# Kernel optimization log

Hardware: AMD Instinct MI355X
Metric: run time of the kernel (lower is better)

The kernel has to match this reference:

```python
import jax, jax.numpy as jnp
import numpy as np

EPS = 1e-6      # mLSTM normalizer epsilon
LN_EPS = 1e-5   # LayerNorm epsilon (equinox default)
S, E, NH = 2048, 1024, 8
DH = E // NH


def setup_inputs() -> dict:
    key = jax.random.key(0)
    ks = jax.random.split(key, 7)
    q = jax.random.normal(ks[0], (S, E), jnp.float32)
    k = jax.random.normal(ks[1], (S, E), jnp.float32)
    v = jax.random.normal(ks[2], (S, E), jnp.float32)
    # Gate projections: Linear(3E -> NH). Module inits weights to zero; we use
    # small random weights so the S x S gate structure is data-dependent and the
    # full math path is exercised. Biases follow the module's init scheme.
    igate_w = 0.02 * jax.random.normal(ks[3], (NH, 3 * E), jnp.float32)
    igate_b = jnp.linspace(3.0, 6.0, NH, dtype=jnp.float32)
    fgate_w = 0.02 * jax.random.normal(ks[4], (NH, 3 * E), jnp.float32)
    fgate_b = jnp.sqrt(jnp.float32(0.1)) * jax.random.normal(ks[5], (NH,), jnp.float32)
    ln_w = jnp.ones((E,), jnp.float32)  # outnorm weight (use_bias=False)
    return {"q": q, "k": k, "v": v, "igate_w": igate_w, "igate_b": igate_b,
            "fgate_w": fgate_w, "fgate_b": fgate_b, "ln_w": ln_w}


def _mlstm_forward(q, k, v, igate_w, igate_b, fgate_w, fgate_b, ln_w):
    s, e = q.shape
    nh = igate_b.shape[0]
    dh = e // nh
    # gate preactivations from concatenated q,k,v: [S, 3E] @ [3E, NH] -> [NH, S]
    x = jnp.concatenate([q, k, v], axis=1)
    ig = (x @ igate_w.T + igate_b).T            # [NH, S]
    fg = (x @ fgate_w.T + fgate_b).T            # [NH, S]
    # split heads: [NH, S, DH]
    qh = q.reshape(s, nh, dh).transpose(1, 0, 2)
    kh = k.reshape(s, nh, dh).transpose(1, 0, 2)
    vh = v.reshape(s, nh, dh).transpose(1, 0, 2)
    # log forget gates and cumulative sums (with leading zero)
    logf = jax.nn.log_sigmoid(fg)                                   # [NH, S]
    cs = jnp.concatenate([jnp.zeros((nh, 1), logf.dtype),
                          jnp.cumsum(logf, axis=1)], axis=1)        # [NH, S+1]
    # log_fg_matrix[h,i,j] = cs[h,i+1] - cs[h,j+1], masked to causal
    dlog = cs[:, 1:, None] - cs[:, None, 1:]                        # [NH, S, S]
    mask = jnp.tril(jnp.ones((s, s), dtype=bool))
    log_fg_matrix = jnp.where(mask, dlog, -jnp.inf)
    # log D = log forget decay + input gate preact (per source position j)
    log_D = log_fg_matrix + ig[:, None, :]                          # [NH, S, S]
    max_log_D = jnp.max(log_D, axis=-1, keepdims=True)              # row-wise stabilization
    D = jnp.exp(log_D - max_log_D)
    qk = jnp.einsum("hsd,htd->hst", qh, kh) / jnp.sqrt(jnp.float32(dh))
    C = qk * D
    normalizer = jnp.maximum(jnp.abs(C.sum(axis=-1, keepdims=True)), jnp.exp(-max_log_D))
    h = jnp.einsum("hst,htd->hsd", C / (normalizer + EPS), vh)      # [NH, S, DH]
    h = h.transpose(1, 0, 2).reshape(s, e)
    # outnorm: LayerNorm over embedding dim, weight only (no bias)
    mu = h.mean(axis=-1, keepdims=True)
    var = ((h - mu) ** 2).mean(axis=-1, keepdims=True)
    return (h - mu) / jnp.sqrt(var + LN_EPS) * ln_w


def reference(q, k, v, igate_w, igate_b, fgate_w, fgate_b, ln_w):
    return _mlstm_forward(q, k, v, igate_w, igate_b, fgate_w, fgate_b, ln_w)
```

## Files before the change

kernel.cpp:

```cpp
#include <hip/hip_runtime.h>
#include <hip/hip_bf16.h>
#include <math.h>

#define S_LEN 2048
#define E_DIM 1024
#define NHEAD 8
#define DHEAD 128
#define MEPS 1e-6f
#define LNEPS 1e-5f
#define TASKS_PER_HEAD 61

typedef __bf16 bf16x8 __attribute__((ext_vector_type(8)));
typedef __bf16 bf16x4 __attribute__((ext_vector_type(4)));
typedef float f32x4 __attribute__((ext_vector_type(4)));
typedef float f32x16 __attribute__((ext_vector_type(16)));

__device__ __host__ inline int ns_of(int qg) { return (4 * qg + 13) / 10; }

__device__ inline void split8(const float* x, bf16x8& hi, bf16x8& lo) {
#pragma unroll
  for (int e = 0; e < 8; ++e) {
    float v = x[e];
    __bf16 h = (__bf16)v;
    hi[e] = h;
    lo[e] = (__bf16)(v - (float)h);
  }
}

__device__ inline int cvtpk(float a, float b) {
  int d;
  asm("v_cvt_pk_bf16_f32 %0, %1, %2" : "=v"(d) : "v"(a), "v"(b));
  return d;
}

__global__ __launch_bounds__(256) void convw_kernel(
    const float* __restrict__ k, const float* __restrict__ v,
    const float* __restrict__ igw, const float* __restrict__ fgw,
    __bf16* __restrict__ KfH, __bf16* __restrict__ KfL, __bf16* __restrict__ VT,
    __bf16* __restrict__ WfH, __bf16* __restrict__ WfL) {
  __shared__ float Kl[32][132], Vl[32][132];
  int t = threadIdx.x;
  if (blockIdx.x >= 512) {
    int slot = (blockIdx.x - 512) * 256 + t;
    int f = slot >> 6, l = slot & 63;
    int c = l & 15;
    int koff = f * 32 + (l >> 4) * 8;
    const float* wrow = (c < 8) ? (igw + c * 3072) : (fgw + (c - 8) * 3072);
    float buf[8];
#pragma unroll
    for (int e = 0; e < 8; ++e) buf[e] = wrow[koff + e];
    bf16x8 fh, fl; split8(buf, fh, fl);
    *(bf16x8*)(WfH + (size_t)slot * 8) = fh;
    *(bf16x8*)(WfL + (size_t)slot * 8) = fl;
    return;
  }
  int h = blockIdx.x >> 6, kvt = blockIdx.x & 63;
  int kvbase = kvt * 32;
#pragma unroll
  for (int it = 0; it < 4; ++it) {
    int fid = it * 256 + t;
    int r = fid >> 5, c4 = (fid & 31) * 4;
    *(float4*)&Kl[r][c4] = *(const float4*)(k + (size_t)(kvbase + r) * E_DIM + h * DHEAD + c4);
    *(float4*)&Vl[r][c4] = *(const float4*)(v + (size_t)(kvbase + r) * E_DIM + h * DHEAD + c4);
  }
  __syncthreads();
  size_t tb = (size_t)(h * 64 + kvt) * 4096;
#pragma unroll
  for (int it = 0; it < 2; ++it) {
    int slot = it * 256 + t;
    int f = slot >> 6, l = slot & 63;
    int l31 = l & 31, hi = l >> 5;
    {
      float buf[8];
#pragma unroll
      for (int e = 0; e < 8; ++e) buf[e] = Kl[l31][f * 16 + hi * 8 + e];
      bf16x8 fh, fl; split8(buf, fh, fl);
      *(bf16x8*)(KfH + tb + (size_t)slot * 8) = fh;
      *(bf16x8*)(KfL + tb + (size_t)slot * 8) = fl;
    }
    {
      int dt = f >> 1, kch = f & 1;
      bf16x8 fh;
#pragma unroll
      for (int e = 0; e < 8; ++e) fh[e] = (__bf16)Vl[kch * 16 + hi * 8 + e][dt * 32 + l31];
      *(bf16x8*)(VT + tb + (size_t)slot * 8) = fh;
    }
  }
}

__global__ __launch_bounds__(256) void gates_mfma_kernel(
    const float* __restrict__ q, const float* __restrict__ k, const float* __restrict__ v,
    const __bf16* __restrict__ WfH, const __bf16* __restrict__ WfL,
    float* __restrict__ gpart) {
  int rb = blockIdx.x >> 3;
  int ks = blockIdx.x & 7;
  int r0 = rb * 64;
  int tid = threadIdx.x, wave = tid >> 6, lane = tid & 63;
  int l15 = lane & 15, hi = lane >> 4;
  __shared__ char Xl[64 * 512];

  f32x4 cacc = (f32x4){0.f, 0.f, 0.f, 0.f};
  for (int ch = 0; ch < 3; ++ch) {
    int kb = ks * 384 + ch * 128;
    __syncthreads();
#pragma unroll
    for (int it = 0; it < 8; ++it) {
      int fid = it * 256 + tid;
      int row = fid >> 5, c4 = (fid & 31) * 4;
      int kk = kb + c4;
      const float* src = (kk < 1024) ? (q + (size_t)(r0 + row) * 1024 + kk)
                       : (kk < 2048) ? (k + (size_t)(r0 + row) * 1024 + (kk - 1024))
                                     : (v + (size_t)(r0 + row) * 1024 + (kk - 2048));
      float4 xv = *(const float4*)src;
      *(float4*)(Xl + ((row * 512 + c4 * 4) ^ ((row & 7) << 4))) = xv;
    }
    __syncthreads();
#pragma unroll
    for (int kc = 0; kc < 4; ++kc) {
      int row = wave * 16 + l15;
      int base = row * 512 + (kc * 32 + hi * 8) * 4;
      int x = (row & 7) << 4;
      float buf[8];
      *(float4*)&buf[0] = *(const float4*)(Xl + (base ^ x));
      *(float4*)&buf[4] = *(const float4*)(Xl + ((base + 16) ^ x));
      bf16x8 ah, al; split8(buf, ah, al);
      int gkc = ks * 12 + ch * 4 + kc;
      bf16x8 bh = *(const bf16x8*)(WfH + (size_t)(gkc * 64 + lane) * 8);
      bf16x8 bl = *(const bf16x8*)(WfL + (size_t)(gkc * 64 + lane) * 8);
      cacc = __builtin_amdgcn_mfma_f32_16x16x32_bf16(ah, bh, cacc, 0, 0, 0);
      cacc = __builtin_amdgcn_mfma_f32_16x16x32_bf16(ah, bl, cacc, 0, 0, 0);
      cacc = __builtin_amdgcn_mfma_f32_16x16x32_bf16(al, bh, cacc, 0, 0, 0);
    }
  }
#pragma unroll
  for (int rg = 0; rg < 4; ++rg) {
    int r = r0 + wave * 16 + hi * 4 + rg;
    gpart[((size_t)ks * S_LEN + r) * 16 + l15] = cacc[rg];
  }
}

__global__ __launch_bounds__(256) void combine_ls_kernel(
    const float* __restrict__ gpart, const float* __restrict__ igb,
    const float* __restrict__ fgb, float* __restrict__ ig, double* __restrict__ ls) {
  int t = blockIdx.x * 256 + threadIdx.x;
  int r = t >> 4, c = t & 15;
  float s = 0.f;
#pragma unroll
  for (int ks = 0; ks < 8; ++ks) s += gpart[((size_t)ks * S_LEN + r) * 16 + c];
  if (c < 8) {
    ig[c * S_LEN + r] = s + igb[c];
  } else {
    double x = (double)(s + fgb[c - 8]);
    ls[(c - 8) * S_LEN + r] = fmin(x, 0.0) - log1p(exp(-fabs(x)));
  }
}

__global__ void scan_kernel(const float* __restrict__ ig, const double* __restrict__ ls,
                            double* __restrict__ g, double* __restrict__ Mv,
                            float* __restrict__ rexpv) {
  int h = blockIdx.x;
  int lane = threadIdx.x;
  double cs0[32];
  const double* lsp = ls + h * S_LEN + lane * 32;
  double run = 0.0;
#pragma unroll
  for (int e = 0; e < 32; ++e) { run += lsp[e]; cs0[e] = run; }
  double incl = run;
#pragma unroll
  for (int off = 1; off < 64; off <<= 1) {
    double nb = __shfl_up(incl, off);
    if (lane >= off) incl += nb;
  }
  double base = __shfl_up(incl, 1);
  if (lane == 0) base = 0.0;
#pragma unroll
  for (int e = 0; e < 32; ++e) cs0[e] += base;

  const float* igp = ig + h * S_LEN + lane * 32;
  double gv[32];
#pragma unroll
  for (int e = 0; e < 32; ++e) {
    gv[e] = (double)igp[e] - cs0[e];
    g[h * S_LEN + lane * 32 + e] = gv[e];
  }
  double pm = -INFINITY;
#pragma unroll
  for (int e = 0; e < 32; ++e) { pm = fmax(pm, gv[e]); gv[e] = pm; }
  double inclm = pm;
#pragma unroll
  for (int off = 1; off < 64; off <<= 1) {
    double nb = __shfl_up(inclm, off);
    if (lane >= off) inclm = fmax(inclm, nb);
  }
  double basem = __shfl_up(inclm, 1);
  if (lane == 0) basem = -INFINITY;
#pragma unroll
  for (int e = 0; e < 32; ++e) {
    double Mi = fmax(basem, gv[e]);
    Mv[h * S_LEN + lane * 32 + e] = Mi;
    rexpv[h * S_LEN + lane * 32 + e] = __expf(-(float)(cs0[e] + Mi));
  }
}

__global__ __launch_bounds__(256) void rebase_kernel(
    const double* __restrict__ g, const double* __restrict__ Mv,
    float* __restrict__ gq, float* __restrict__ Mq) {
  const double L2E = 1.4426950408889634;
  int b = blockIdx.x;
  int h = b >> 4, qg = b & 15;
  int tid = threadIdx.x;
  double base = Mv[h * S_LEN + qg * 128];
#pragma unroll
  for (int it = 0; it < 8; ++it) {
    int j = it * 256 + tid;
    gq[(size_t)(h * 16 + qg) * S_LEN + j] = (float)((g[h * S_LEN + j] - base) * L2E);
  }
  if (tid < 128) {
    int i = qg * 128 + tid;
    Mq[h * S_LEN + i] = (float)((Mv[h * S_LEN + i] - base) * L2E);
  }
}

__global__ __launch_bounds__(256, 2) void attn_kernel(
    const float* __restrict__ q,
    const __bf16* __restrict__ KfH, const __bf16* __restrict__ KfL,
    const __bf16* __restrict__ VT,
    const float* __restrict__ gq, const float* __restrict__ Mq,
    __bf16* __restrict__ part, float* __restrict__ bpart) {
  int rem = blockIdx.x;
  int qg = 15, preLow = 0, ns = 1;
  for (int qq = 15; qq >= 0; --qq) {
    int n = ns_of(qq);
    if (rem < 8 * n) { qg = qq; ns = n; break; }
    rem -= 8 * n;
  }
  for (int qq = 0; qq < qg; ++qq) preLow += ns_of(qq);
  int h = rem & 7;
  int split = rem >> 3;
  int T = 4 * qg + 4;
  int kb_lo = (split * T) / ns;
  int kb_hi = ((split + 1) * T) / ns;
  int Tq = kb_hi - kb_lo;
  int tid = threadIdx.x, wave = tid >> 6, lane = tid & 63;
  int l31 = lane & 31, hi = lane >> 5;
  const float scale = 0.08838834764831845f;

  __shared__ char smem[49152];

  int qrow = qg * 128 + wave * 32 + l31;
  bf16x8 qfh[8], qfl[8];
  {
    const float* qp = q + (size_t)qrow * E_DIM + h * DHEAD + hi * 8;
#pragma unroll
    for (int kch = 0; kch < 8; ++kch) {
      float buf[8];
      *(float4*)&buf[0] = *(const float4*)(qp + kch * 16);
      *(float4*)&buf[4] = *(const float4*)(qp + kch * 16 + 4);
#pragma unroll
      for (int e = 0; e < 8; ++e) buf[e] *= scale;
      split8(buf, qfh[kch], qfl[kch]);
    }
  }
  float Mreg = Mq[h * S_LEN + qrow];
  const float* gqh = gq + (size_t)(h * 16 + qg) * S_LEN;

  f32x16 acc[4];
#pragma unroll
  for (int dt = 0; dt < 4; ++dt) acc[dt] = (f32x16)(0.f);
  float bacc = 0.f;

  size_t laneoff = (size_t)lane * 8;
  auto STAGE = [&](int kb, int buf) {
    size_t tb = (size_t)(h * 64 + kb) * 4096;
    char* lb = smem + buf * 24576;
#pragma unroll
    for (int i = 0; i < 6; ++i) {
      int c = wave * 6 + i;
      const __bf16* src;
      if (c < 8)       src = KfH + tb + (size_t)c * 512 + laneoff;
      else if (c < 16) src = KfL + tb + (size_t)(c - 8) * 512 + laneoff;
      else             src = VT  + tb + (size_t)(c - 16) * 512 + laneoff;
      __builtin_amdgcn_global_load_lds(
          (const __attribute__((address_space(1))) void*)src,
          (__attribute__((address_space(3))) void*)(lb + c * 1024), 16, 0, 0);
    }
  };

  if (Tq > 0) STAGE(kb_lo, 0);
  int cur = 0;
  for (int t = 0; t < Tq; ++t) {
    int kb = kb_lo + t;
    asm volatile("s_waitcnt vmcnt(0)" ::: "memory");
    __builtin_amdgcn_sched_barrier(0);
    asm volatile("s_barrier" ::: "memory");
    if (t + 1 < Tq) STAGE(kb + 1, cur ^ 1);

    int qrelw = qg * 128 + wave * 32 - kb * 32;
    if (qrelw + 31 >= 0) {
      char* lb = smem + cur * 24576;
      int qrel = qrelw + l31;
      float4 g4[4];
#pragma unroll
      for (int c = 0; c < 4; ++c) g4[c] = *(const float4*)(gqh + kb * 32 + 8 * c + 4 * hi);
      f32x16 sA = (f32x16)(0.f), sB = (f32x16)(0.f), sC = (f32x16)(0.f);
      __builtin_amdgcn_s_setprio(1);
#pragma unroll
      for (int kch = 0; kch < 8; ++kch) {
        bf16x8 kh = *(const bf16x8*)(lb + kch * 1024 + lane * 16);
        bf16x8 kl = *(const bf16x8*)(lb + 8192 + kch * 1024 + lane * 16);
        sA = __builtin_amdgcn_mfma_f32_32x32x16_bf16(kh, qfh[kch], sA, 0, 0, 0);
        sB = __builtin_amdgcn_mfma_f32_32x32x16_bf16(kl, qfh[kch], sB, 0, 0, 0);
        sC = __builtin_amdgcn_mfma_f32_32x32x16_bf16(kh, qfl[kch], sC, 0, 0, 0);
      }
      __builtin_amdgcn_s_setprio(0);
      float p[16];
      float bp0 = 0.f, bp1 = 0.f, bp2 = 0.f, bp3 = 0.f;
      if (qrelw >= 31) {
#pragma unroll
        for (int rg = 0; rg < 16; ++rg) {
          float sv = sA[rg] + sB[rg] + sC[rg];
          p[rg] = sv * exp2f(((const float*)&g4[rg >> 2])[rg & 3] - Mreg);
          if ((rg & 3) == 0) bp0 += p[rg];
          else if ((rg & 3) == 1) bp1 += p[rg];
          else if ((rg & 3) == 2) bp2 += p[rg];
          else bp3 += p[rg];
        }
      } else {
#pragma unroll
        for (int rg = 0; rg < 16; ++rg) {
          int J = (rg & 3) + 8 * (rg >> 2) + 4 * hi;
          float sv = sA[rg] + sB[rg] + sC[rg];
          float w = sv * exp2f(((const float*)&g4[rg >> 2])[rg & 3] - Mreg);
          p[rg] = (J <= qrel) ? w : 0.f;
          if ((rg & 3) == 0) bp0 += p[rg];
          else if ((rg & 3) == 1) bp1 += p[rg];
          else if ((rg & 3) == 2) bp2 += p[rg];
          else bp3 += p[rg];
        }
      }
      bacc += (bp0 + bp1) + (bp2 + bp3);
#pragma unroll
      for (int kch = 0; kch < 2; ++kch) {
        const float* pp = p + kch * 8;
        int a0 = cvtpk(pp[0], pp[1]);
        int a1 = cvtpk(pp[2], pp[3]);
        int a2 = cvtpk(pp[4], pp[5]);
        int a3 = cvtpk(pp[6], pp[7]);
        asm("v_permlane32_swap_b32 %0, %1" : "+v"(a0), "+v"(a2));
        asm("v_permlane32_swap_b32 %0, %1" : "+v"(a1), "+v"(a3));
        union { int w[4]; bf16x8 v; } pb;
        pb.w[0] = a0; pb.w[1] = a1; pb.w[2] = a2; pb.w[3] = a3;
        __builtin_amdgcn_s_setprio(1);
#pragma unroll
        for (int dt = 0; dt < 4; ++dt) {
          bf16x8 va = *(const bf16x8*)(lb + 16384 + (dt * 2 + kch) * 1024 + lane * 16);
          acc[dt] = __builtin_amdgcn_mfma_f32_32x32x16_bf16(va, pb.v, acc[dt], 0, 0, 0);
        }
        __builtin_amdgcn_s_setprio(0);
      }
    }
    cur ^= 1;
  }

  {
    int x = __float_as_int(bacc), y = x;
    asm("v_permlane32_swap_b32 %0, %1" : "+v"(x), "+v"(y));
    float bfull = __int_as_float(x) + __int_as_float(y);
    int task = h * TASKS_PER_HEAD + preLow + split;
    if (lane < 32) bpart[task * 128 + wave * 32 + lane] = bfull;

    __syncthreads();
    char* Tls = smem + wave * 8704;
#pragma unroll
    for (int dt = 0; dt < 4; ++dt)
#pragma unroll
      for (int rgq = 0; rgq < 4; ++rgq) {
        bf16x4 pk;
        pk[0] = (__bf16)acc[dt][rgq * 4 + 0];
        pk[1] = (__bf16)acc[dt][rgq * 4 + 1];
        pk[2] = (__bf16)acc[dt][rgq * 4 + 2];
        pk[3] = (__bf16)acc[dt][rgq * 4 + 3];
        int d0 = dt * 32 + rgq * 8 + hi * 4;
        *(bf16x4*)(Tls + l31 * 272 + d0 * 2) = pk;
      }
    __syncthreads();
    __bf16* pp = part + (size_t)task * 16384;
#pragma unroll
    for (int it = 0; it < 8; ++it) {
      int qr = it * 4 + (lane >> 4);
      int chunk = lane & 15;
      bf16x8 vrow = *(const bf16x8*)(Tls + qr * 272 + chunk * 16);
      *(bf16x8*)(pp + ((size_t)(wave * 32 + qr) * 128 + chunk * 8)) = vrow;
    }
  }
}

__global__ __launch_bounds__(256) void cln_kernel(
    const __bf16* __restrict__ part, const float* __restrict__ bpart,
    const float* __restrict__ rexpv, const float* __restrict__ lnw,
    float* __restrict__ out) {
  int b = blockIdx.x;
  int qg = b >> 4, slab = b & 15;
  int ns = ns_of(qg);
  int preLow = 0;
  for (int qq = 0; qq < qg; ++qq) preLow += ns_of(qq);
  int tid = threadIdx.x;
  int tokl = tid >> 5;
  int j = tid & 31;
  int qv = slab * 8 + tokl;
  int tok = qg * 128 + qv;
  int h = j >> 2;
  int d0 = (j & 3) * 32;
  int task0 = h * TASKS_PER_HEAD + preLow;

  float a[32];
#pragma unroll
  for (int i = 0; i < 32; ++i) a[i] = 0.f;
  float bb = 0.f;
  for (int s = 0; s < ns; ++s) {
    const __bf16* pp = part + (size_t)(task0 + s) * 16384 + qv * 128 + d0;
#pragma unroll
    for (int c = 0; c < 4; ++c) {
      bf16x8 xv = *(const bf16x8*)(pp + c * 8);
#pragma unroll
      for (int e = 0; e < 8; ++e) a[c * 8 + e] += (float)xv[e];
    }
    bb += bpart[(task0 + s) * 128 + qv];
  }
  float norm = fmaxf(fabsf(bb), rexpv[h * S_LEN + tok]) + MEPS;
  float inv = 1.f / norm;
  float sum = 0.f, sq = 0.f;
#pragma unroll
  for (int i = 0; i < 32; ++i) {
    a[i] *= inv;
    sum += a[i];
    sq += a[i] * a[i];
  }
#pragma unroll
  for (int off = 1; off < 32; off <<= 1) {
    sum += __shfl_xor(sum, off);
    sq  += __shfl_xor(sq, off);
  }
  float mu = sum * (1.f / E_DIM);
  float var = sq * (1.f / E_DIM) - mu * mu;
  float rstd = rsqrtf(var + LNEPS);
  float* dst = out + (size_t)tok * E_DIM + j * 32;
  const float* wsrc = lnw + j * 32;
#pragma unroll
  for (int c = 0; c < 8; ++c) {
    float4 w = *(const float4*)(wsrc + c * 4);
    float4 o;
    o.x = (a[c * 4 + 0] - mu) * rstd * w.x;
    o.y = (a[c * 4 + 1] - mu) * rstd * w.y;
    o.z = (a[c * 4 + 2] - mu) * rstd * w.z;
    o.w = (a[c * 4 + 3] - mu) * rstd * w.w;
    *(float4*)(dst + c * 4) = o;
  }
}

extern "C" void kernel_launch(void* const* d_in, const int* in_sizes, int n_in,
                              void* d_out, int out_size, void* d_ws, size_t ws_size,
                              hipStream_t stream) {
  const float* q   = (const float*)d_in[0];
  const float* k   = (const float*)d_in[1];
  const float* v   = (const float*)d_in[2];
  const float* igw = (const float*)d_in[3];
  const float* igb = (const float*)d_in[4];
  const float* fgw = (const float*)d_in[5];
  const float* fgb = (const float*)d_in[6];
  const float* lnw = (const float*)d_in[7];
  float* out = (float*)d_out;

  const size_t MB = 1024 * 1024;
  char* base = (char*)d_ws;
  float*  ig    = (float*)(base + 0);
  float*  rexpv = (float*)(base + 64 * 1024);
  float*  Mq    = (float*)(base + 128 * 1024);
  float*  bpart = (float*)(base + 192 * 1024);
  double* ls    = (double*)(base + 704 * 1024);
  double* g64   = (double*)(base + 832 * 1024);
  double* M64   = (double*)(base + 960 * 1024);
  __bf16* WfH   = (__bf16*)(base + 1088 * 1024);
  __bf16* WfL   = (__bf16*)(base + 1184 * 1024);
  float*  gq    = (float*)(base + 1536 * 1024);
  __bf16* KfH   = (__bf16*)(base + 3 * MB);
  __bf16* KfL   = (__bf16*)(base + 7 * MB);
  __bf16* VT    = (__bf16*)(base + 11 * MB);
  __bf16* part  = (__bf16*)(base + 15 * MB);
  float*  gpart = (float*)(base + 31 * MB);

  int nblocks = 8 * TASKS_PER_HEAD;

  convw_kernel<<<dim3(536), dim3(256), 0, stream>>>(k, v, igw, fgw, KfH, KfL, VT, WfH, WfL);
  gates_mfma_kernel<<<dim3(256), dim3(256), 0, stream>>>(q, k, v, WfH, WfL, gpart);
  combine_ls_kernel<<<dim3(128), dim3(256), 0, stream>>>(gpart, igb, fgb, ig, ls);
  scan_kernel<<<dim3(NHEAD), dim3(64), 0, stream>>>(ig, ls, g64, M64, rexpv);
  rebase_kernel<<<dim3(128), dim3(256), 0, stream>>>(g64, M64, gq, Mq);
  attn_kernel<<<dim3(nblocks), dim3(256), 0, stream>>>(q, KfH, KfL, VT, gq, Mq, part, bpart);
  cln_kernel<<<dim3(256), dim3(256), 0, stream>>>(part, bpart, rexpv, lnw, out);
}
```

Before: 77.05 us.

## Fuse scan and rebase kernels and increase attention key-split granularity

Merges the per-head prefix scan and the per-query-group rebase into one kernel that keeps cumulative sums and running maxima in shared memory, dropping a launch and the double-precision global round trip. It also changes the split-count formula so the attention kernel uses more tasks per head, raising parallelism at the cost of more partial results to combine. The partial buffer offset is moved to make room. The fused kernel runs only 8 blocks writing all gq rows, which may serialize work that was previously spread over 128 blocks.

```diff
diff --git a/kernel.cpp b/kernel.cpp
--- a/kernel.cpp
+++ b/kernel.cpp
@@ -8,14 +8,14 @@
 #define DHEAD 128
 #define MEPS 1e-6f
 #define LNEPS 1e-5f
-#define TASKS_PER_HEAD 61
+#define TASKS_PER_HEAD 72
 
 typedef __bf16 bf16x8 __attribute__((ext_vector_type(8)));
 typedef __bf16 bf16x4 __attribute__((ext_vector_type(4)));
 typedef float f32x4 __attribute__((ext_vector_type(4)));
 typedef float f32x16 __attribute__((ext_vector_type(16)));
 
-__device__ __host__ inline int ns_of(int qg) { return (4 * qg + 13) / 10; }
+__device__ __host__ inline int ns_of(int qg) { return (4 * qg + 11) / 8; }
 
 __device__ inline void split8(const float* x, bf16x8& hi, bf16x8& lo) {
 #pragma unroll
@@ -155,69 +155,73 @@
   }
 }
 
-__global__ void scan_kernel(const float* __restrict__ ig, const double* __restrict__ ls,
-                            double* __restrict__ g, double* __restrict__ Mv,
-                            float* __restrict__ rexpv) {
+__global__ __launch_bounds__(256) void scanreb_kernel(
+    const float* __restrict__ ig, const double* __restrict__ ls,
+    float* __restrict__ gq, float* __restrict__ Mq, float* __restrict__ rexpv) {
   int h = blockIdx.x;
-  int lane = threadIdx.x;
-  double cs0[32];
-  const double* lsp = ls + h * S_LEN + lane * 32;
-  double run = 0.0;
-#pragma unroll
-  for (int e = 0; e < 32; ++e) { run += lsp[e]; cs0[e] = run; }
-  double incl = run;
-#pragma unroll
-  for (int off = 1; off < 64; off <<= 1) {
-    double nb = __shfl_up(incl, off);
-    if (lane >= off) incl += nb;
-  }
-  double base = __shfl_up(incl, 1);
-  if (lane == 0) base = 0.0;
-#pragma unroll
-  for (int e = 0; e < 32; ++e) cs0[e] += base;
-
-  const float* igp = ig + h * S_LEN + lane * 32;
-  double gv[32];
-#pragma unroll
-  for (int e = 0; e < 32; ++e) {
-    gv[e] = (double)igp[e] - cs0[e];
-    g[h * S_LEN + lane * 32 + e] = gv[e];
-  }
-  double pm = -INFINITY;
-#pragma unroll
-  for (int e = 0; e < 32; ++e) { pm = fmax(pm, gv[e]); gv[e] = pm; }
-  double inclm = pm;
-#pragma unroll
-  for (int off = 1; off < 64; off <<= 1) {
-    double nb = __shfl_up(inclm, off);
-    if (lane >= off) inclm = fmax(inclm, nb);
-  }
-  double basem = __shfl_up(inclm, 1);
-  if (lane == 0) basem = -INFINITY;
-#pragma unroll
-  for (int e = 0; e < 32; ++e) {
-    double Mi = fmax(basem, gv[e]);
-    Mv[h * S_LEN + lane * 32 + e] = Mi;
-    rexpv[h * S_LEN + lane * 32 + e] = __expf(-(float)(cs0[e] + Mi));
-  }
-}
-
-__global__ __launch_bounds__(256) void rebase_kernel(
-    const double* __restrict__ g, const double* __restrict__ Mv,
-    float* __restrict__ gq, float* __restrict__ Mq) {
+  int tid = threadIdx.x;
+  __shared__ double Lg[2048];
+  __shared__ double Lcs[2048];
+  __shared__ double LM[2048];
+
+  if (tid < 64) {
+    int lane = tid;
+    double cs0[32];
+    const double* lsp = ls + h * S_LEN + lane * 32;
+    double run = 0.0;
+#pragma unroll
+    for (int e = 0; e < 32; ++e) { run += lsp[e]; cs0[e] = run; }
+    double incl = run;
+#pragma unroll
+    for (int off = 1; off < 64; off <<= 1) {
+      double nb = __shfl_up(incl, off);
+      if (lane >= off) incl += nb;
+    }
+    double base = __shfl_up(incl, 1);
+    if (lane == 0) base = 0.0;
+#pragma unroll
+    for (int e = 0; e < 32; ++e) cs0[e] += base;
+
+    const float* igp = ig + h * S_LEN + lane * 32;
+    double gv[32];
+#pragma unroll
+    for (int e = 0; e < 32; ++e) {
+      gv[e] = (double)igp[e] - cs0[e];
+      Lg[lane * 32 + e] = gv[e];
+      Lcs[lane * 32 + e] = cs0[e];
+    }
+    double pm = -INFINITY;
+#pragma unroll
+    for (int e = 0; e < 32; ++e) { pm = fmax(pm, gv[e]); gv[e] = pm; }
+    double inclm = pm;
+#pragma unroll
+    for (int off = 1; off < 64; off <<= 1) {
+      double nb = __shfl_up(inclm, off);
+      if (lane >= off) inclm = fmax(inclm, nb);
+    }
+    double basem = __shfl_up(inclm, 1);
+    if (lane == 0) basem = -INFINITY;
+#pragma unroll
+    for (int e = 0; e < 32; ++e) LM[lane * 32 + e] = fmax(basem, gv[e]);
+  }
+  __syncthreads();
+
   const double L2E = 1.4426950408889634;
-  int b = blockIdx.x;
-  int h = b >> 4, qg = b & 15;
-  int tid = threadIdx.x;
-  double base = Mv[h * S_LEN + qg * 128];
 #pragma unroll
   for (int it = 0; it < 8; ++it) {
-    int j = it * 256 + tid;
-    gq[(size_t)(h * 16 + qg) * S_LEN + j] = (float)((g[h * S_LEN + j] - base) * L2E);
-  }
-  if (tid < 128) {
-    int i = qg * 128 + tid;
-    Mq[h * S_LEN + i] = (float)((Mv[h * S_LEN + i] - base) * L2E);
+    int i = it * 256 + tid;
+    int qgi = i >> 7;
+    Mq[h * S_LEN + i] = (float)((LM[i] - LM[qgi * 128]) * L2E);
+    rexpv[h * S_LEN + i] = __expf(-(float)(Lcs[i] + LM[i]));
+  }
+  for (int qg = 0; qg < 16; ++qg) {
+    double base = LM[qg * 128];
+    float* dst = gq + (size_t)(h * 16 + qg) * S_LEN;
+#pragma unroll
+    for (int it = 0; it < 8; ++it) {
+      int j = it * 256 + tid;
+      dst[j] = (float)((Lg[j] - base) * L2E);
+    }
   }
 }
 
@@ -478,8 +482,6 @@
   float*  Mq    = (float*)(base + 128 * 1024);
   float*  bpart = (float*)(base + 192 * 1024);
   double* ls    = (double*)(base + 704 * 1024);
-  double* g64   = (double*)(base + 832 * 1024);
-  double* M64   = (double*)(base + 960 * 1024);
   __bf16* WfH   = (__bf16*)(base + 1088 * 1024);
   __bf16* WfL   = (__bf16*)(base + 1184 * 1024);
   float*  gq    = (float*)(base + 1536 * 1024);
@@ -487,15 +489,14 @@
   __bf16* KfL   = (__bf16*)(base + 7 * MB);
   __bf16* VT    = (__bf16*)(base + 11 * MB);
   __bf16* part  = (__bf16*)(base + 15 * MB);
-  float*  gpart = (float*)(base + 31 * MB);
+  float*  gpart = (float*)(base + 33 * MB);
 
   int nblocks = 8 * TASKS_PER_HEAD;
 
   convw_kernel<<<dim3(536), dim3(256), 0, stream>>>(k, v, igw, fgw, KfH, KfL, VT, WfH, WfL);
   gates_mfma_kernel<<<dim3(256), dim3(256), 0, stream>>>(q, k, v, WfH, WfL, gpart);
   combine_ls_kernel<<<dim3(128), dim3(256), 0, stream>>>(gpart, igb, fgb, ig, ls);
-  scan_kernel<<<dim3(NHEAD), dim3(64), 0, stream>>>(ig, ls, g64, M64, rexpv);
-  rebase_kernel<<<dim3(128), dim3(256), 0, stream>>>(g64, M64, gq, Mq);
+  scanreb_kernel<<<dim3(NHEAD), dim3(256), 0, stream>>>(ig, ls, gq, Mq, rexpv);
   attn_kernel<<<dim3(nblocks), dim3(256), 0, stream>>>(q, KfH, KfL, VT, gq, Mq, part, bpart);
   cln_kernel<<<dim3(256), dim3(256), 0, stream>>>(part, bpart, rexpv, lnw, out);
 }
```

Measured after the change: 79.63 us. 3.3% more time.
